# Kernel optimization log

Hardware: AMD Instinct MI355X
Metric: run time of the kernel (lower is better)

The kernel has to match this reference:

```python
import jax, jax.numpy as jnp
import numpy as np

NB_STEPS = 50
ALPHA = 0.9
NUM_RNN_STEPS = 2
B = 4096
NUM_FEATURE = 100
IN_D = 5
HIDDEN = [64, 64, 64]
P1 = (1.1, 1.1, 1.5, 2.0, 2.5)   # IntegrandNN_outer_level powers
P2 = (1.5, 2.0, 2.5, 3.0, 3.5)   # IntegrandNN powers


def _cc(nb_steps):
    # Clenshaw-Curtis weights/steps, identical to UMNN's compute_cc_weights
    n = nb_steps
    i = np.arange(n + 1, dtype=np.float64).reshape(-1, 1)
    lam = np.cos(i @ i.T * np.pi / n)
    lam[:, 0] = 0.5
    lam[:, -1] *= 0.5
    lam = lam * 2.0 / n
    W = np.zeros(n + 1)
    even = np.arange(0, n + 1, 2)
    W[even] = 2.0 / (1.0 - even.astype(np.float64) ** 2)
    W[0] = 1.0
    ccw = (lam.T @ W).astype(np.float32)                         # [n+1]
    steps = np.cos(np.arange(n + 1) * np.pi / n).astype(np.float32)  # [n+1]
    return jnp.asarray(ccw), jnp.asarray(steps)

CC_W, CC_S = _cc(NB_STEPS)


def _mlp(xh, Ws, bs):
    # Linear+ReLU stack with ELU on the last layer (ReLU popped, ELU appended)
    h = xh
    for W, b in zip(Ws[:-1], bs[:-1]):
        h = jax.nn.relu(h @ W.T + b)
    return jax.nn.elu(h @ Ws[-1].T + bs[-1])


def _integrand(x, h, Ws, bs, Wf, powers):
    z = _mlp(jnp.concatenate([x, h], axis=1), Ws, bs) + 1.0      # [N,1], z >= 0
    feats = jnp.concatenate([z ** p for p in powers], axis=1)    # [N,5]
    return jax.nn.relu((1.0 / (feats + 1.0)) @ Wf.T)             # [N,1]


def _integrate(x0, xT, h, f):
    # ParallelNeuralIntegral forward: CC quadrature of f from x0 to xT
    Bn, S = x0.shape[0], NB_STEPS + 1
    X = x0[:, None, :] + (xT - x0)[:, None, :] * (CC_S[None, :, None] + 1.0) / 2.0  # [B,S,1]
    hs = jnp.broadcast_to(h[:, None, :], (Bn, S, h.shape[1])).reshape(-1, h.shape[1])
    dz = f(X.reshape(-1, 1), hs).reshape(Bn, S, 1)
    return (dz * CC_W[None, :, None]).sum(1) * (xT - x0) / 2.0   # [B,1]


def setup_inputs() -> dict:
    key = jax.random.key(0)
    ks = jax.random.split(key, 24)
    def lin(k, o, i):
        return jax.random.normal(k, (o, i), jnp.float32) / np.sqrt(i)
    d = {}
    d["x_"] = jax.random.normal(ks[0], (B, NUM_FEATURE), jnp.float32)
    d["h_"] = jax.random.normal(ks[1], (B, IN_D - 1), jnp.float32)
    d["log_weight"] = jnp.ones((1, NUM_FEATURE), jnp.float32)     # reset_parameters -> 1
    d["sigmoid_param"] = jnp.zeros((1,), jnp.float32)
    sizes = [IN_D] + HIDDEN + [1]
    for tag, base in (("f1", 2), ("f2", 12)):
        for li, (i, o) in enumerate(zip(sizes[:-1], sizes[1:])):
            d[f"{tag}_W{li}"] = lin(ks[base + 2 * li], o, i)
            d[f"{tag}_b{li}"] = jnp.zeros((o,), jnp.float32)
        d[f"{tag}_Wf"] = jnp.abs(lin(ks[base + 9], 1, 5))         # reset_params -> abs
    return d


def reference(x_, h_, log_weight, sigmoid_param,
              f1_W0, f1_b0, f1_W1, f1_b1, f1_W2, f1_b2, f1_W3, f1_b3, f1_Wf,
              f2_W0, f2_b0, f2_W1, f2_b1, f2_W2, f2_b2, f2_W3, f2_b3, f2_Wf):
    f1Ws = [f1_W0, f1_W1, f1_W2, f1_W3]; f1bs = [f1_b0, f1_b1, f1_b2, f1_b3]
    f2Ws = [f2_W0, f2_W1, f2_W2, f2_W3]; f2bs = [f2_b0, f2_b1, f2_b2, f2_b3]
    f1 = lambda x, h: _integrand(x, h, f1Ws, f1bs, f1_Wf, P1)
    f2 = lambda x, h: _integrand(x, h, f2Ws, f2bs, f2_Wf, P2)

    # modular function: linear to [B,1] then sum over dim 1 -> [B,1]
    xm = jnp.sum(x_ * log_weight[0], axis=1, keepdims=True)
    lam = jax.nn.sigmoid(sigmoid_param[0])

    I1 = jnp.zeros_like(xm)
    I2 = jnp.zeros_like(xm)
    out_first = None
    for _ in range(NUM_RNN_STEPS):
        x = (1.0 - lam) * xm + lam * I1
        x2 = (1.0 - lam) * xm + lam * I2
        out_first = f1(x2, h_)
        I1 = _integrate(jnp.zeros_like(x), x, h_, f1)
        xmax = jnp.max(x2) + 10.0
        xfinal = jnp.zeros_like(x) + xmax
        I2 = (1.0 / ALPHA) * _integrate(x2, xfinal, h_, f2)
    return I1, out_first, I2
```

## Files before the change

### kernel.cpp

```cpp
#include <hip/hip_runtime.h>
#include <math.h>

typedef _Float16 half8v __attribute__((ext_vector_type(8)));
typedef _Float16 half4v __attribute__((ext_vector_type(4)));
typedef float float4v __attribute__((ext_vector_type(4)));

#define BB    4096
#define NS    51
#define TBR   5
#define NBI   820
#define NBF   16
#define GRID_INT (2*NBI + NBF)
#define INV_ALPHA (1.0f/0.9f)

#define WS_CCW 0
#define WS_CCS 64
#define WS_LAM 128
#define WS_KEY 132
#define WS_PM  144
#define WS_XM  512
#define WS_X   (WS_XM + BB)
#define WS_X2  (WS_X + BB)
#define WS_H   16384
#define H_NET  8192
#define H_W2   4096
#define H_W0   16384
#define H_W3   20480

#if defined(__has_builtin)
#if __has_builtin(__builtin_amdgcn_rcpf)
#define FRCP(x) __builtin_amdgcn_rcpf(x)
#endif
#endif
#ifndef FRCP
#define FRCP(x) (1.0f / (x))
#endif

__device__ __forceinline__ unsigned fkey(float f) {
    int i = __float_as_int(f);
    return (i >= 0) ? ((unsigned)i + 0x80000000u) : ~(unsigned)i;
}
__device__ __forceinline__ float fkey_inv(unsigned k) {
    return (k & 0x80000000u) ? __int_as_float((int)(k - 0x80000000u))
                             : __int_as_float((int)~k);
}

__device__ __forceinline__ int swz(int row, int cb) {
    return (row << 6) + (((cb ^ (row & 7)) & 7) << 3);
}

__global__ void k_setup(const float* __restrict__ x_, const float* __restrict__ lw,
                        const float* __restrict__ sp,
                        const float* __restrict__ f1W0, const float* __restrict__ f1W1,
                        const float* __restrict__ f1W2, const float* __restrict__ f1W3,
                        const float* __restrict__ f2W0, const float* __restrict__ f2W1,
                        const float* __restrict__ f2W2, const float* __restrict__ f2W3,
                        float* __restrict__ ws) {
    _Float16* wh = (_Float16*)(ws + WS_H);
    const int blk = blockIdx.x, tid = threadIdx.x;
    if (blk < 256) {
        int wave = tid >> 6, lane = tid & 63;
        float vmax = -1e30f;
        for (int r = 0; r < 4; ++r) {
            int row = blk * 16 + wave * 4 + r;
            float v = 0.0f;
            for (int i = lane; i < 100; i += 64) v = fmaf(x_[row * 100 + i], lw[i], v);
            #pragma unroll
            for (int off = 32; off > 0; off >>= 1) v += __shfl_xor(v, off, 64);
            if (lane == 0) ws[WS_XM + row] = v;
            vmax = fmaxf(vmax, v);
        }
        __shared__ float sm[4];
        if (lane == 0) sm[wave] = vmax;
        __syncthreads();
        if (tid == 0)
            ws[WS_PM + blk] = fmaxf(fmaxf(sm[0], sm[1]), fmaxf(sm[2], sm[3]));
    } else if (blk < 272) {
        int t = (blk - 256) * 256 + tid;
        wh[t]                = (_Float16)f1W1[t];
        wh[H_W2 + t]         = (_Float16)f1W2[t];
        wh[H_NET + t]        = (_Float16)f2W1[t];
        wh[H_NET + H_W2 + t] = (_Float16)f2W2[t];
        if (t < 2048) {
            int j = t >> 5, k = t & 31;
            wh[H_W0 + t]        = (k < 5) ? (_Float16)f1W0[j * 5 + k] : (_Float16)0.0f;
            wh[H_W0 + 2048 + t] = (k < 5) ? (_Float16)f2W0[j * 5 + k] : (_Float16)0.0f;
        }
        if (t < 64) {
            wh[H_W3 + t]      = (_Float16)f1W3[t];
            wh[H_W3 + 64 + t] = (_Float16)f2W3[t];
        }
    } else {
        if (tid == 60) ws[WS_LAM] = 1.0f / (1.0f + expf(-sp[0]));
        if (tid == 61) ((unsigned*)ws)[WS_KEY] = 0u;
        if (tid <= 50) {
            ws[WS_CCS + tid] = cospif((float)tid / 50.0f);
            float acc = 0.0f;
            for (int a = 0; a <= 50; ++a) {
                float w;
                if (a == 0) w = 1.0f;
                else if ((a & 1) == 0) w = 2.0f / (1.0f - (float)(a * a));
                else continue;
                float l;
                if (tid == 0) l = 0.5f;
                else {
                    int m = (a * tid) % 100;
                    l = cospif((float)m / 50.0f);
                    if (tid == 50) l *= 0.5f;
                }
                acc += l * 0.04f * w;
            }
            ws[WS_CCW + tid] = acc;
        }
    }
}

__device__ __forceinline__ void mfma_hidden(
    const _Float16* __restrict__ Wg, const float* __restrict__ Bg,
    _Float16* act, int tid)
{
    const int lane = tid & 63, wbase = tid & 192;
    const int lo = lane & 15, quad = lane >> 4;
    half8v Af[4][2];
    #pragma unroll
    for (int m = 0; m < 4; ++m)
        #pragma unroll
        for (int kb = 0; kb < 2; ++kb)
            Af[m][kb] = *(const half8v*)(Wg + (16 * m + lo) * 64 + 32 * kb + quad * 8);
    float4v bb[4];
    #pragma unroll
    for (int m = 0; m < 4; ++m) bb[m] = *(const float4v*)(Bg + 16 * m + quad * 4);
    half8v Bf[4][2];
    #pragma unroll
    for (int n = 0; n < 4; ++n)
        #pragma unroll
        for (int kb = 0; kb < 2; ++kb)
            Bf[n][kb] = *(const half8v*)(act + swz(wbase + 16 * n + lo, 4 * kb + quad));
    float4v accv[4][4];
    #pragma unroll
    for (int m = 0; m < 4; ++m)
        #pragma unroll
        for (int n = 0; n < 4; ++n) {
            float4v c = bb[m];
            c = __builtin_amdgcn_mfma_f32_16x16x32_f16(Af[m][0], Bf[n][0], c, 0, 0, 0);
            c = __builtin_amdgcn_mfma_f32_16x16x32_f16(Af[m][1], Bf[n][1], c, 0, 0, 0);
            accv[m][n] = c;
        }
    #pragma unroll
    for (int m = 0; m < 4; ++m)
        #pragma unroll
        for (int n = 0; n < 4; ++n) {
            float4v c = accv[m][n];
            half4v o;
            o[0] = (_Float16)fmaxf(c[0], 0.0f); o[1] = (_Float16)fmaxf(c[1], 0.0f);
            o[2] = (_Float16)fmaxf(c[2], 0.0f); o[3] = (_Float16)fmaxf(c[3], 0.0f);
            *(half4v*)(act + swz(wbase + 16 * n + lo, 2 * m + (quad >> 1)) + 4 * (quad & 1)) = o;
        }
}

__device__ __forceinline__ void mfma_first(
    const _Float16* __restrict__ Wg, const float* __restrict__ Bg,
    _Float16* act, int tid)
{
    const int lane = tid & 63, wbase = tid & 192;
    const int lo = lane & 15, quad = lane >> 4;
    half8v Af[4];
    #pragma unroll
    for (int m = 0; m < 4; ++m)
        Af[m] = *(const half8v*)(Wg + (16 * m + lo) * 32 + quad * 8);
    float4v bb[4];
    #pragma unroll
    for (int m = 0; m < 4; ++m) bb[m] = *(const float4v*)(Bg + 16 * m + quad * 4);
    half8v Bf[4];
    #pragma unroll
    for (int n = 0; n < 4; ++n)
        Bf[n] = *(const half8v*)(act + swz(wbase + 16 * n + lo, quad));
    float4v accv[4][4];
    #pragma unroll
    for (int m = 0; m < 4; ++m)
        #pragma unroll
        for (int n = 0; n < 4; ++n)
            accv[m][n] = __builtin_amdgcn_mfma_f32_16x16x32_f16(Af[m], Bf[n], bb[m], 0, 0, 0);
    #pragma unroll
    for (int m = 0; m < 4; ++m)
        #pragma unroll
        for (int n = 0; n < 4; ++n) {
            float4v c = accv[m][n];
            half4v o;
            o[0] = (_Float16)fmaxf(c[0], 0.0f); o[1] = (_Float16)fmaxf(c[1], 0.0f);
            o[2] = (_Float16)fmaxf(c[2], 0.0f); o[3] = (_Float16)fmaxf(c[3], 0.0f);
            *(half4v*)(act + swz(wbase + 16 * n + lo, 2 * m + (quad >> 1)) + 4 * (quad & 1)) = o;
        }
}

__global__ __launch_bounds__(256) void k_int(
    int mode, float* __restrict__ ws, const float* __restrict__ h_,
    const float* __restrict__ f1b0, const float* __restrict__ f1b1,
    const float* __restrict__ f1b2, const float* __restrict__ f1b3,
    const float* __restrict__ f1Wf,
    const float* __restrict__ f2b0, const float* __restrict__ f2b1,
    const float* __restrict__ f2b2, const float* __restrict__ f2b3,
    const float* __restrict__ f2Wf,
    float* __restrict__ out)
{
    __shared__ _Float16 act[256 * 64];
    float* red = (float*)act;

    const int blk = blockIdx.x, tid = threadIdx.x;
    const float* xm = ws + WS_XM;
    const float* xarr = ws + WS_X;
    const float* x2arr = ws + WS_X2;
    const _Float16* wh = (const _Float16*)(ws + WS_H);
    const float lam = ws[WS_LAM];
    const float oml = 1.0f - lam;

    int kind, b_base = 0, b, s = 0;
    if (blk < NBI)          { kind = 0; b_base = blk * TBR; }
    else if (blk < 2 * NBI) { kind = 1; b_base = (blk - NBI) * TBR; }
    else                    { kind = 2; }

    float xmax = 0.0f, xin;
    if (kind == 2) {
        b = (blk - 2 * NBI) * 256 + tid;
        xin = mode ? x2arr[b] : oml * xm[b];
    } else {
        if (kind == 1) {
            if (mode) {
                xmax = fkey_inv(((const unsigned*)ws)[WS_KEY]) + 10.0f;
            } else {
                int lane = tid & 63;
                const float* pm = ws + WS_PM;
                float v = fmaxf(fmaxf(pm[lane], pm[lane + 64]),
                                fmaxf(pm[lane + 128], pm[lane + 192]));
                #pragma unroll
                for (int off = 32; off > 0; off >>= 1) v = fmaxf(v, __shfl_xor(v, off, 64));
                xmax = oml * v + 10.0f;
            }
        }
        int lb = tid / 51;
        s = tid - lb * 51;
        b = b_base + (lb < TBR - 1 ? lb : TBR - 1);
        if (b > BB - 1) b = BB - 1;
        float t = (ws[WS_CCS + s] + 1.0f) * 0.5f;
        if (kind == 0) {
            float xb = mode ? xarr[b] : oml * xm[b];
            xin = xb * t;
        } else {
            float x0v = mode ? x2arr[b] : oml * xm[b];
            xin = x0v + (xmax - x0v) * t;
        }
    }
    const float4 h4 = ((const float4*)h_)[b];

    const bool u2 = (kind == 1);
    const _Float16* W0h = wh + H_W0 + (u2 ? 2048 : 0);
    const _Float16* W1h = wh + (u2 ? H_NET : 0);
    const _Float16* W2h = W1h + H_W2;
    const _Float16* W3h = wh + H_W3 + (u2 ? 64 : 0);
    const float* B0 = u2 ? f2b0 : f1b0;
    const float* B1 = u2 ? f2b1 : f1b1;
    const float* B2 = u2 ? f2b2 : f1b2;
    const float* B3 = u2 ? f2b3 : f1b3;
    const float* WF = u2 ? f2Wf : f1Wf;
    const float p0 = u2 ? 1.5f : 1.1f;
    const float p1 = u2 ? 2.0f : 1.1f;
    const float p2 = u2 ? 2.5f : 1.5f;
    const float p3 = u2 ? 3.0f : 2.0f;
    const float p4 = u2 ? 3.5f : 2.5f;

    {
        half8v sv;
        sv[0] = (_Float16)xin; sv[1] = (_Float16)h4.x; sv[2] = (_Float16)h4.y;
        sv[3] = (_Float16)h4.z; sv[4] = (_Float16)h4.w;
        sv[5] = (_Float16)0.0f; sv[6] = (_Float16)0.0f; sv[7] = (_Float16)0.0f;
        half8v zv;
        #pragma unroll
        for (int e = 0; e < 8; ++e) zv[e] = (_Float16)0.0f;
        *(half8v*)(act + swz(tid, 0)) = sv;
        *(half8v*)(act + swz(tid, 1)) = zv;
        *(half8v*)(act + swz(tid, 2)) = zv;
        *(half8v*)(act + swz(tid, 3)) = zv;
    }

    mfma_first (W0h, B0, act, tid);
    mfma_hidden(W1h, B1, act, tid);
    mfma_hidden(W2h, B2, act, tid);

    float y = B3[0];
    #pragma unroll
    for (int g = 0; g < 8; ++g) {
        half8v hv = *(const half8v*)(act + swz(tid, g));
        half8v wv = *(const half8v*)(W3h + 8 * g);
        #pragma unroll
        for (int e = 0; e < 8; ++e) y = fmaf((float)wv[e], (float)hv[e], y);
    }
    if (y <= 0.0f) y = __expf(y) - 1.0f;
    float z = y + 1.0f;
    float lg = __logf(z);
    float g = WF[0] * FRCP(__expf(p0 * lg) + 1.0f)
            + WF[1] * FRCP(__expf(p1 * lg) + 1.0f)
            + WF[2] * FRCP(__expf(p2 * lg) + 1.0f)
            + WF[3] * FRCP(__expf(p3 * lg) + 1.0f)
            + WF[4] * FRCP(__expf(p4 * lg) + 1.0f);
    float val = fmaxf(g, 0.0f);

    if (kind == 2) { out[BB + b] = val; return; }

    __syncthreads();
    red[tid] = ws[WS_CCW + s] * val;
    __syncthreads();

    if (kind == 0) {
        if (tid < TBR) {
            float sum = 0.0f;
            for (int i = 0; i < NS; ++i) sum += red[tid * NS + i];
            int bo = b_base + tid;
            if (bo < BB) {
                float xb = mode ? xarr[bo] : oml * xm[bo];
                float I1 = sum * xb * 0.5f;
                out[bo] = I1;
                if (!mode) ws[WS_X + bo] = oml * xm[bo] + lam * I1;
            }
        }
    } else {
        float x2n = -3e38f;
        if (tid < TBR) {
            float sum = 0.0f;
            for (int i = 0; i < NS; ++i) sum += red[tid * NS + i];
            int bo = b_base + tid;
            if (bo < BB) {
                float x2b = mode ? x2arr[bo] : oml * xm[bo];
                float I2 = sum * (xmax - x2b) * 0.5f * INV_ALPHA;
                out[2 * BB + bo] = I2;
                if (!mode) {
                    x2n = oml * xm[bo] + lam * I2;
                    ws[WS_X2 + bo] = x2n;
                }
            }
        }
        if (!mode && tid < 64) {
            #pragma unroll
            for (int off = 32; off > 0; off >>= 1)
                x2n = fmaxf(x2n, __shfl_xor(x2n, off, 64));
            if (tid == 0) atomicMax((unsigned*)ws + WS_KEY, fkey(x2n));
        }
    }
}

extern "C" void kernel_launch(void* const* d_in, const int* in_sizes, int n_in,
                              void* d_out, int out_size, void* d_ws, size_t ws_size,
                              hipStream_t stream) {
    const float* x_  = (const float*)d_in[0];
    const float* h_  = (const float*)d_in[1];
    const float* lw  = (const float*)d_in[2];
    const float* sp  = (const float*)d_in[3];
    const float* f1W0 = (const float*)d_in[4];   const float* f1b0 = (const float*)d_in[5];
    const float* f1W1 = (const float*)d_in[6];   const float* f1b1 = (const float*)d_in[7];
    const float* f1W2 = (const float*)d_in[8];   const float* f1b2 = (const float*)d_in[9];
    const float* f1W3 = (const float*)d_in[10];  const float* f1b3 = (const float*)d_in[11];
    const float* f1Wf = (const float*)d_in[12];
    const float* f2W0 = (const float*)d_in[13];  const float* f2b0 = (const float*)d_in[14];
    const float* f2W1 = (const float*)d_in[15];  const float* f2b1 = (const float*)d_in[16];
    const float* f2W2 = (const float*)d_in[17];  const float* f2b2 = (const float*)d_in[18];
    const float* f2W3 = (const float*)d_in[19];  const float* f2b3 = (const float*)d_in[20];
    const float* f2Wf = (const float*)d_in[21];
    float* out = (float*)d_out;
    float* ws  = (float*)d_ws;

    k_setup<<<273, 256, 0, stream>>>(x_, lw, sp,
                                     f1W0, f1W1, f1W2, f1W3,
                                     f2W0, f2W1, f2W2, f2W3, ws);
    k_int<<<GRID_INT, 256, 0, stream>>>(0, ws, h_,
        f1b0, f1b1, f1b2, f1b3, f1Wf, f2b0, f2b1, f2b2, f2b3, f2Wf, out);
    k_int<<<GRID_INT, 256, 0, stream>>>(1, ws, h_,
        f1b0, f1b1, f1b2, f1b3, f1Wf, f2b0, f2b1, f2b2, f2b3, f2Wf, out);
}
```

Measured before the change: 162.6 us.

## Map one wavefront per batch row and reduce quadrature with shuffles

The integration kernel now launches 64-thread blocks, each handling one batch row with its 51 quadrature points padded to 64 lanes. The first-layer input is built directly in MFMA B-fragment registers, and the last layer is a register dot product plus cross-lane shuffles instead of an LDS round trip. The quadrature sum uses wave shuffles instead of two block barriers and a serial shared-memory sum. The global max key is spread over 64 atomic slots, and the out_first blocks run only in the second pass. This removes barriers and cuts LDS use from 32KB to 8KB per block, which should help occupancy, but padding 51 to 64 wastes more MFMA lanes than the previous 5-rows-per-256 packing.

```diff
diff --git a/kernel.cpp b/kernel.cpp
--- a/kernel.cpp
+++ b/kernel.cpp
@@ -7,25 +7,21 @@
 
 #define BB    4096
 #define NS    51
-#define TBR   5
-#define NBI   820
-#define NBF   16
-#define GRID_INT (2*NBI + NBF)
 #define INV_ALPHA (1.0f/0.9f)
 
-#define WS_CCW 0
-#define WS_CCS 64
-#define WS_LAM 128
-#define WS_KEY 132
-#define WS_PM  144
-#define WS_XM  512
-#define WS_X   (WS_XM + BB)
-#define WS_X2  (WS_X + BB)
-#define WS_H   16384
-#define H_NET  8192
-#define H_W2   4096
-#define H_W0   16384
-#define H_W3   20480
+#define WS_CCW   0
+#define WS_CCS   64
+#define WS_LAM   128
+#define WS_KEY64 160
+#define WS_PM    256
+#define WS_XM    512
+#define WS_X     (WS_XM + BB)
+#define WS_X2    (WS_X + BB)
+#define WS_H     16384
+#define H_NET    8192
+#define H_W2     4096
+#define H_W0     16384
+#define H_W3     20480
 
 #if defined(__has_builtin)
 #if __has_builtin(__builtin_amdgcn_rcpf)
@@ -91,10 +87,11 @@
             wh[H_W3 + 64 + t] = (_Float16)f2W3[t];
         }
     } else {
-        if (tid == 60) ws[WS_LAM] = 1.0f / (1.0f + expf(-sp[0]));
-        if (tid == 61) ((unsigned*)ws)[WS_KEY] = 0u;
-        if (tid <= 50) {
-            ws[WS_CCS + tid] = cospif((float)tid / 50.0f);
+        if (tid < 64) ((unsigned*)ws)[WS_KEY64 + tid] = 0u;
+        if (tid == 64) ws[WS_LAM] = 1.0f / (1.0f + expf(-sp[0]));
+        if (tid >= 128 && tid <= 178) {
+            int s = tid - 128;
+            ws[WS_CCS + s] = cospif((float)s / 50.0f);
             float acc = 0.0f;
             for (int a = 0; a <= 50; ++a) {
                 float w;
@@ -102,98 +99,20 @@
                 else if ((a & 1) == 0) w = 2.0f / (1.0f - (float)(a * a));
                 else continue;
                 float l;
-                if (tid == 0) l = 0.5f;
+                if (s == 0) l = 0.5f;
                 else {
-                    int m = (a * tid) % 100;
+                    int m = (a * s) % 100;
                     l = cospif((float)m / 50.0f);
-                    if (tid == 50) l *= 0.5f;
+                    if (s == 50) l *= 0.5f;
                 }
                 acc += l * 0.04f * w;
             }
-            ws[WS_CCW + tid] = acc;
-        }
-    }
-}
-
-__device__ __forceinline__ void mfma_hidden(
-    const _Float16* __restrict__ Wg, const float* __restrict__ Bg,
-    _Float16* act, int tid)
-{
-    const int lane = tid & 63, wbase = tid & 192;
-    const int lo = lane & 15, quad = lane >> 4;
-    half8v Af[4][2];
-    #pragma unroll
-    for (int m = 0; m < 4; ++m)
-        #pragma unroll
-        for (int kb = 0; kb < 2; ++kb)
-            Af[m][kb] = *(const half8v*)(Wg + (16 * m + lo) * 64 + 32 * kb + quad * 8);
-    float4v bb[4];
-    #pragma unroll
-    for (int m = 0; m < 4; ++m) bb[m] = *(const float4v*)(Bg + 16 * m + quad * 4);
-    half8v Bf[4][2];
-    #pragma unroll
-    for (int n = 0; n < 4; ++n)
-        #pragma unroll
-        for (int kb = 0; kb < 2; ++kb)
-            Bf[n][kb] = *(const half8v*)(act + swz(wbase + 16 * n + lo, 4 * kb + quad));
-    float4v accv[4][4];
-    #pragma unroll
-    for (int m = 0; m < 4; ++m)
-        #pragma unroll
-        for (int n = 0; n < 4; ++n) {
-            float4v c = bb[m];
-            c = __builtin_amdgcn_mfma_f32_16x16x32_f16(Af[m][0], Bf[n][0], c, 0, 0, 0);
-            c = __builtin_amdgcn_mfma_f32_16x16x32_f16(Af[m][1], Bf[n][1], c, 0, 0, 0);
-            accv[m][n] = c;
-        }
-    #pragma unroll
-    for (int m = 0; m < 4; ++m)
-        #pragma unroll
-        for (int n = 0; n < 4; ++n) {
-            float4v c = accv[m][n];
-            half4v o;
-            o[0] = (_Float16)fmaxf(c[0], 0.0f); o[1] = (_Float16)fmaxf(c[1], 0.0f);
-            o[2] = (_Float16)fmaxf(c[2], 0.0f); o[3] = (_Float16)fmaxf(c[3], 0.0f);
-            *(half4v*)(act + swz(wbase + 16 * n + lo, 2 * m + (quad >> 1)) + 4 * (quad & 1)) = o;
-        }
-}
-
-__device__ __forceinline__ void mfma_first(
-    const _Float16* __restrict__ Wg, const float* __restrict__ Bg,
-    _Float16* act, int tid)
-{
-    const int lane = tid & 63, wbase = tid & 192;
-    const int lo = lane & 15, quad = lane >> 4;
-    half8v Af[4];
-    #pragma unroll
-    for (int m = 0; m < 4; ++m)
-        Af[m] = *(const half8v*)(Wg + (16 * m + lo) * 32 + quad * 8);
-    float4v bb[4];
-    #pragma unroll
-    for (int m = 0; m < 4; ++m) bb[m] = *(const float4v*)(Bg + 16 * m + quad * 4);
-    half8v Bf[4];
-    #pragma unroll
-    for (int n = 0; n < 4; ++n)
-        Bf[n] = *(const half8v*)(act + swz(wbase + 16 * n + lo, quad));
-    float4v accv[4][4];
-    #pragma unroll
-    for (int m = 0; m < 4; ++m)
-        #pragma unroll
-        for (int n = 0; n < 4; ++n)
-            accv[m][n] = __builtin_amdgcn_mfma_f32_16x16x32_f16(Af[m], Bf[n], bb[m], 0, 0, 0);
-    #pragma unroll
-    for (int m = 0; m < 4; ++m)
-        #pragma unroll
-        for (int n = 0; n < 4; ++n) {
-            float4v c = accv[m][n];
-            half4v o;
-            o[0] = (_Float16)fmaxf(c[0], 0.0f); o[1] = (_Float16)fmaxf(c[1], 0.0f);
-            o[2] = (_Float16)fmaxf(c[2], 0.0f); o[3] = (_Float16)fmaxf(c[3], 0.0f);
-            *(half4v*)(act + swz(wbase + 16 * n + lo, 2 * m + (quad >> 1)) + 4 * (quad & 1)) = o;
-        }
-}
-
-__global__ __launch_bounds__(256) void k_int(
+            ws[WS_CCW + s] = acc;
+        }
+    }
+}
+
+__global__ __launch_bounds__(64) void k_int(
     int mode, float* __restrict__ ws, const float* __restrict__ h_,
     const float* __restrict__ f1b0, const float* __restrict__ f1b1,
     const float* __restrict__ f1b2, const float* __restrict__ f1b3,
@@ -203,10 +122,12 @@
     const float* __restrict__ f2Wf,
     float* __restrict__ out)
 {
-    __shared__ _Float16 act[256 * 64];
-    float* red = (float*)act;
-
-    const int blk = blockIdx.x, tid = threadIdx.x;
+    __shared__ _Float16 act[64 * 64];
+
+    const int blk = blockIdx.x;
+    const int lane = threadIdx.x;
+    const int lo = lane & 15, q = lane >> 4;
+
     const float* xm = ws + WS_XM;
     const float* xarr = ws + WS_X;
     const float* x2arr = ws + WS_X2;
@@ -214,43 +135,33 @@
     const float lam = ws[WS_LAM];
     const float oml = 1.0f - lam;
 
-    int kind, b_base = 0, b, s = 0;
-    if (blk < NBI)          { kind = 0; b_base = blk * TBR; }
-    else if (blk < 2 * NBI) { kind = 1; b_base = (blk - NBI) * TBR; }
-    else                    { kind = 2; }
-
-    float xmax = 0.0f, xin;
-    if (kind == 2) {
-        b = (blk - 2 * NBI) * 256 + tid;
-        xin = mode ? x2arr[b] : oml * xm[b];
-    } else {
-        if (kind == 1) {
-            if (mode) {
-                xmax = fkey_inv(((const unsigned*)ws)[WS_KEY]) + 10.0f;
-            } else {
-                int lane = tid & 63;
-                const float* pm = ws + WS_PM;
-                float v = fmaxf(fmaxf(pm[lane], pm[lane + 64]),
-                                fmaxf(pm[lane + 128], pm[lane + 192]));
-                #pragma unroll
-                for (int off = 32; off > 0; off >>= 1) v = fmaxf(v, __shfl_xor(v, off, 64));
-                xmax = oml * v + 10.0f;
-            }
-        }
-        int lb = tid / 51;
-        s = tid - lb * 51;
-        b = b_base + (lb < TBR - 1 ? lb : TBR - 1);
-        if (b > BB - 1) b = BB - 1;
-        float t = (ws[WS_CCS + s] + 1.0f) * 0.5f;
-        if (kind == 0) {
-            float xb = mode ? xarr[b] : oml * xm[b];
-            xin = xb * t;
+    int kind, b = 0, b0 = 0;
+    if (blk < 4096)      { kind = 0; b = blk; }
+    else if (blk < 8192) { kind = 1; b = blk - 4096; }
+    else                 { kind = 2; b0 = (blk - 8192) * 64; b = b0 + lane; }
+
+    float xmax = 0.0f, xb = 0.0f, x0 = 0.0f;
+    float4 h4u = {0, 0, 0, 0};
+    if (kind == 0) {
+        xb = mode ? xarr[b] : oml * xm[b];
+        h4u = ((const float4*)h_)[b];
+    } else if (kind == 1) {
+        if (mode) {
+            float v = fkey_inv(((const unsigned*)ws)[WS_KEY64 + lane]);
+            #pragma unroll
+            for (int off = 32; off > 0; off >>= 1) v = fmaxf(v, __shfl_xor(v, off, 64));
+            xmax = v + 10.0f;
         } else {
-            float x0v = mode ? x2arr[b] : oml * xm[b];
-            xin = x0v + (xmax - x0v) * t;
-        }
-    }
-    const float4 h4 = ((const float4*)h_)[b];
+            const float* pm = ws + WS_PM;
+            float v = fmaxf(fmaxf(pm[lane], pm[lane + 64]),
+                            fmaxf(pm[lane + 128], pm[lane + 192]));
+            #pragma unroll
+            for (int off = 32; off > 0; off >>= 1) v = fmaxf(v, __shfl_xor(v, off, 64));
+            xmax = oml * v + 10.0f;
+        }
+        x0 = mode ? x2arr[b] : oml * xm[b];
+        h4u = ((const float4*)h_)[b];
+    }
 
     const bool u2 = (kind == 1);
     const _Float16* W0h = wh + H_W0 + (u2 ? 2048 : 0);
@@ -268,32 +179,124 @@
     const float p3 = u2 ? 3.0f : 2.0f;
     const float p4 = u2 ? 3.5f : 2.5f;
 
+    float4v accv[4][4];
+
     {
-        half8v sv;
-        sv[0] = (_Float16)xin; sv[1] = (_Float16)h4.x; sv[2] = (_Float16)h4.y;
-        sv[3] = (_Float16)h4.z; sv[4] = (_Float16)h4.w;
-        sv[5] = (_Float16)0.0f; sv[6] = (_Float16)0.0f; sv[7] = (_Float16)0.0f;
-        half8v zv;
-        #pragma unroll
-        for (int e = 0; e < 8; ++e) zv[e] = (_Float16)0.0f;
-        *(half8v*)(act + swz(tid, 0)) = sv;
-        *(half8v*)(act + swz(tid, 1)) = zv;
-        *(half8v*)(act + swz(tid, 2)) = zv;
-        *(half8v*)(act + swz(tid, 3)) = zv;
-    }
-
-    mfma_first (W0h, B0, act, tid);
-    mfma_hidden(W1h, B1, act, tid);
-    mfma_hidden(W2h, B2, act, tid);
-
-    float y = B3[0];
+        half8v Bf0[4];
+        #pragma unroll
+        for (int n = 0; n < 4; ++n) {
+            int r = 16 * n + lo;
+            float xr; float4 hr;
+            if (kind == 2) {
+                int idx = b0 + r;
+                xr = x2arr[idx];
+                hr = ((const float4*)h_)[idx];
+            } else {
+                int si = r > 50 ? 50 : r;
+                float t = (ws[WS_CCS + si] + 1.0f) * 0.5f;
+                xr = (kind == 0) ? xb * t : x0 + (xmax - x0) * t;
+                hr = h4u;
+            }
+            half8v e;
+            e[0] = (_Float16)xr; e[1] = (_Float16)hr.x; e[2] = (_Float16)hr.y;
+            e[3] = (_Float16)hr.z; e[4] = (_Float16)hr.w;
+            e[5] = (_Float16)0.0f; e[6] = (_Float16)0.0f; e[7] = (_Float16)0.0f;
+            half8v z;
+            #pragma unroll
+            for (int t2 = 0; t2 < 8; ++t2) z[t2] = (_Float16)0.0f;
+            Bf0[n] = (q == 0) ? e : z;
+        }
+        #pragma unroll
+        for (int m = 0; m < 4; ++m) {
+            half8v Af = *(const half8v*)(W0h + (16 * m + lo) * 32 + q * 8);
+            float4v bb = *(const float4v*)(B0 + 16 * m + q * 4);
+            #pragma unroll
+            for (int n = 0; n < 4; ++n)
+                accv[m][n] = __builtin_amdgcn_mfma_f32_16x16x32_f16(Af, Bf0[n], bb, 0, 0, 0);
+        }
+        #pragma unroll
+        for (int m = 0; m < 4; ++m)
+            #pragma unroll
+            for (int n = 0; n < 4; ++n) {
+                float4v c = accv[m][n];
+                half4v o;
+                o[0] = (_Float16)fmaxf(c[0], 0.0f); o[1] = (_Float16)fmaxf(c[1], 0.0f);
+                o[2] = (_Float16)fmaxf(c[2], 0.0f); o[3] = (_Float16)fmaxf(c[3], 0.0f);
+                *(half4v*)(act + swz(16 * n + lo, 2 * m + (q >> 1)) + 4 * (q & 1)) = o;
+            }
+    }
+
+    {
+        half8v Bf[2][4];
+        #pragma unroll
+        for (int kb = 0; kb < 2; ++kb)
+            #pragma unroll
+            for (int n = 0; n < 4; ++n)
+                Bf[kb][n] = *(const half8v*)(act + swz(16 * n + lo, 4 * kb + q));
+        #pragma unroll
+        for (int m = 0; m < 4; ++m) {
+            float4v bb = *(const float4v*)(B1 + 16 * m + q * 4);
+            half8v A0 = *(const half8v*)(W1h + (16 * m + lo) * 64 + q * 8);
+            half8v A1 = *(const half8v*)(W1h + (16 * m + lo) * 64 + 32 + q * 8);
+            #pragma unroll
+            for (int n = 0; n < 4; ++n) {
+                float4v c = bb;
+                c = __builtin_amdgcn_mfma_f32_16x16x32_f16(A0, Bf[0][n], c, 0, 0, 0);
+                c = __builtin_amdgcn_mfma_f32_16x16x32_f16(A1, Bf[1][n], c, 0, 0, 0);
+                accv[m][n] = c;
+            }
+        }
+        #pragma unroll
+        for (int m = 0; m < 4; ++m)
+            #pragma unroll
+            for (int n = 0; n < 4; ++n) {
+                float4v c = accv[m][n];
+                half4v o;
+                o[0] = (_Float16)fmaxf(c[0], 0.0f); o[1] = (_Float16)fmaxf(c[1], 0.0f);
+                o[2] = (_Float16)fmaxf(c[2], 0.0f); o[3] = (_Float16)fmaxf(c[3], 0.0f);
+                *(half4v*)(act + swz(16 * n + lo, 2 * m + (q >> 1)) + 4 * (q & 1)) = o;
+            }
+    }
+
+    {
+        half8v Bf[2][4];
+        #pragma unroll
+        for (int kb = 0; kb < 2; ++kb)
+            #pragma unroll
+            for (int n = 0; n < 4; ++n)
+                Bf[kb][n] = *(const half8v*)(act + swz(16 * n + lo, 4 * kb + q));
+        #pragma unroll
+        for (int m = 0; m < 4; ++m) {
+            float4v bb = *(const float4v*)(B2 + 16 * m + q * 4);
+            half8v A0 = *(const half8v*)(W2h + (16 * m + lo) * 64 + q * 8);
+            half8v A1 = *(const half8v*)(W2h + (16 * m + lo) * 64 + 32 + q * 8);
+            #pragma unroll
+            for (int n = 0; n < 4; ++n) {
+                float4v c = bb;
+                c = __builtin_amdgcn_mfma_f32_16x16x32_f16(A0, Bf[0][n], c, 0, 0, 0);
+                c = __builtin_amdgcn_mfma_f32_16x16x32_f16(A1, Bf[1][n], c, 0, 0, 0);
+                accv[m][n] = c;
+            }
+        }
+    }
+
+    float part[4] = {0.0f, 0.0f, 0.0f, 0.0f};
     #pragma unroll
-    for (int g = 0; g < 8; ++g) {
-        half8v hv = *(const half8v*)(act + swz(tid, g));
-        half8v wv = *(const half8v*)(W3h + 8 * g);
-        #pragma unroll
-        for (int e = 0; e < 8; ++e) y = fmaf((float)wv[e], (float)hv[e], y);
-    }
+    for (int m = 0; m < 4; ++m) {
+        half4v w3 = *(const half4v*)(W3h + 16 * m + 4 * q);
+        #pragma unroll
+        for (int n = 0; n < 4; ++n)
+            #pragma unroll
+            for (int e = 0; e < 4; ++e)
+                part[n] = fmaf((float)w3[e], fmaxf(accv[m][n][e], 0.0f), part[n]);
+    }
+    #pragma unroll
+    for (int n = 0; n < 4; ++n) {
+        part[n] += __shfl_xor(part[n], 16, 64);
+        part[n] += __shfl_xor(part[n], 32, 64);
+    }
+    float y = B3[0] + (q == 0 ? part[0] : q == 1 ? part[1] : q == 2 ? part[2] : part[3]);
+
     if (y <= 0.0f) y = __expf(y) - 1.0f;
     float z = y + 1.0f;
     float lg = __logf(z);
@@ -306,43 +309,23 @@
 
     if (kind == 2) { out[BB + b] = val; return; }
 
-    __syncthreads();
-    red[tid] = ws[WS_CCW + s] * val;
-    __syncthreads();
-
-    if (kind == 0) {
-        if (tid < TBR) {
-            float sum = 0.0f;
-            for (int i = 0; i < NS; ++i) sum += red[tid * NS + i];
-            int bo = b_base + tid;
-            if (bo < BB) {
-                float xb = mode ? xarr[bo] : oml * xm[bo];
-                float I1 = sum * xb * 0.5f;
-                out[bo] = I1;
-                if (!mode) ws[WS_X + bo] = oml * xm[bo] + lam * I1;
-            }
-        }
-    } else {
-        float x2n = -3e38f;
-        if (tid < TBR) {
-            float sum = 0.0f;
-            for (int i = 0; i < NS; ++i) sum += red[tid * NS + i];
-            int bo = b_base + tid;
-            if (bo < BB) {
-                float x2b = mode ? x2arr[bo] : oml * xm[bo];
-                float I2 = sum * (xmax - x2b) * 0.5f * INV_ALPHA;
-                out[2 * BB + bo] = I2;
-                if (!mode) {
-                    x2n = oml * xm[bo] + lam * I2;
-                    ws[WS_X2 + bo] = x2n;
-                }
-            }
-        }
-        if (!mode && tid < 64) {
-            #pragma unroll
-            for (int off = 32; off > 0; off >>= 1)
-                x2n = fmaxf(x2n, __shfl_xor(x2n, off, 64));
-            if (tid == 0) atomicMax((unsigned*)ws + WS_KEY, fkey(x2n));
+    float c = (lane <= 50) ? ws[WS_CCW + lane] * val : 0.0f;
+    #pragma unroll
+    for (int off = 32; off > 0; off >>= 1) c += __shfl_xor(c, off, 64);
+
+    if (lane == 0) {
+        if (kind == 0) {
+            float I1 = c * xb * 0.5f;
+            out[b] = I1;
+            if (!mode) ws[WS_X + b] = oml * xm[b] + lam * I1;
+        } else {
+            float I2 = c * (xmax - x0) * 0.5f * INV_ALPHA;
+            out[2 * BB + b] = I2;
+            if (!mode) {
+                float x2n = oml * xm[b] + lam * I2;
+                ws[WS_X2 + b] = x2n;
+                atomicMax((unsigned*)ws + WS_KEY64 + (b & 63), fkey(x2n));
+            }
         }
     }
 }
@@ -370,8 +353,8 @@
     k_setup<<<273, 256, 0, stream>>>(x_, lw, sp,
                                      f1W0, f1W1, f1W2, f1W3,
                                      f2W0, f2W1, f2W2, f2W3, ws);
-    k_int<<<GRID_INT, 256, 0, stream>>>(0, ws, h_,
+    k_int<<<8192, 64, 0, stream>>>(0, ws, h_,
         f1b0, f1b1, f1b2, f1b3, f1Wf, f2b0, f2b1, f2b2, f2b3, f2Wf, out);
-    k_int<<<GRID_INT, 256, 0, stream>>>(1, ws, h_,
+    k_int<<<8256, 64, 0, stream>>>(1, ws, h_,
         f1b0, f1b1, f1b2, f1b3, f1Wf, f2b0, f2b1, f2b2, f2b3, f2Wf, out);
 }
```

After: 164.1 us. Within noise of the previous version (+0.9%).
